# Performance work log

Measured on AMD Instinct MI355X. Metric: run time of the kernel, lower is better.

## Reference

```python
import jax, jax.numpy as jnp
import numpy as np


def setup_inputs() -> dict:
    key = jax.random.key(0)
    ks = jax.random.split(key, 9)
    B, T, F_IN = 128, 2048, 32
    R, H, F_OUT = 256, 256, 32
    s = lambda k, shape, fan: jax.random.normal(k, shape, dtype=jnp.float32) * (1.0 / np.sqrt(fan))
    return {
        "input_seq": jax.random.normal(ks[0], (B, T, F_IN), dtype=jnp.float32),
        "enc_W": s(ks[1], (R, F_IN), F_IN),
        "enc_b": s(ks[2], (R,), F_IN),
        "W_ih": s(ks[3], (4 * H, R), H),
        "W_hh": s(ks[4], (4 * H, H), H),
        "b_ih": s(ks[5], (4 * H,), H),
        "b_hh": s(ks[6], (4 * H,), H),
        "dec_W": s(ks[7], (F_OUT, H), H),
        "dec_b": s(ks[8], (F_OUT,), H),
        "future_n": 64,
    }


def reference(input_seq, enc_W, enc_b, W_ih, W_hh, b_ih, b_hh, dec_W, dec_b, future_n):
    # Faithful to source: `state` is never updated inside the loop, so every
    # timestep applies the LSTMCell to the SAME initial state (eval: zeros).
    B, T, _ = input_seq.shape
    H = W_hh.shape[1]
    h0 = jnp.zeros((B, H), dtype=input_seq.dtype)
    c0 = jnp.zeros((B, H), dtype=input_seq.dtype)

    encoded = jnp.einsum('btf,rf->btr', input_seq, enc_W) + enc_b  # [B,T,R]
    # future steps all reuse the last encoded timestep
    last = jnp.broadcast_to(encoded[:, -1:, :], (B, future_n, encoded.shape[-1]))
    enc_full = jnp.concatenate([encoded, last], axis=1)  # [B, T+future_n, R]

    # LSTMCell gates (PyTorch order: i, f, g, o); state contribution is constant.
    state_gates = h0 @ W_hh.T + b_hh  # [B, 4H] (zeros state -> just b_hh)
    gates = jnp.einsum('btr,gr->btg', enc_full, W_ih) + b_ih + state_gates[:, None, :]
    i, f, g, o = jnp.split(gates, 4, axis=-1)
    c = jax.nn.sigmoid(f) * c0[:, None, :] + jax.nn.sigmoid(i) * jnp.tanh(g)
    h = jax.nn.sigmoid(o) * jnp.tanh(c)  # [B, T+future_n, H]

    return jnp.einsum('bth,oh->bto', h, dec_W) + dec_b
```

## Files before the change

kernel.cpp:

```cpp
#include <hip/hip_runtime.h>


typedef _Float16 f16x8 __attribute__((ext_vector_type(8)));
typedef _Float16 f16x4 __attribute__((ext_vector_type(4)));
typedef float    f32x4 __attribute__((ext_vector_type(4)));
typedef _Float16 hx2   __attribute__((ext_vector_type(2)));
typedef __fp16   pk16x2 __attribute__((ext_vector_type(2)));

#define T_IN 2048
#define TT   2112
#define FIN  32
#define FOUT 32

#define WS_FB_OFF   49152
#define WS_DECW_OFF 52224

union PkCast { pk16x2 p; hx2 h; unsigned u; };

__device__ __forceinline__ hx2 pk2(float a, float b) {
    PkCast c; c.p = __builtin_amdgcn_cvt_pkrtz(a, b); return c.h;
}
__device__ __forceinline__ hx2 splat(float v) {
    _Float16 h = (_Float16)v; return (hx2){h, h};
}
__device__ __forceinline__ hx2 pk_rcp(hx2 d, hx2 TWO) {
    union { hx2 h; unsigned u; } a, r;
    a.h = d;
    r.u = 0x78007800u - a.u;
    hx2 y = r.h;
    y = y * (TWO - d * y);
    y = y * (TWO - d * y);
    return y;
}

__global__ __launch_bounds__(256) void prep2(
    const float* __restrict__ enc_W, const float* __restrict__ enc_b,
    const float* __restrict__ W_ih, const float* __restrict__ b_ih,
    const float* __restrict__ b_hh, const float* __restrict__ dec_W,
    _Float16* __restrict__ Mb, float* __restrict__ fb, _Float16* __restrict__ decWb) {
    const int blk = blockIdx.x;
    const int tid = threadIdx.x;
    if (blk < 768) {
        const int gg = blk, sg = gg + (gg >= 256 ? 256 : 0);
        const float scale = (gg >= 256 && gg < 512) ? 0.25f : 0.125f;
        const float* wr = W_ih + (size_t)sg * 256;
        const int f = tid & 31, r8 = tid >> 5;
        float acc = 0.f;
#pragma unroll
        for (int k = 0; k < 32; ++k) {
            int r = r8 * 32 + k;
            acc = fmaf(wr[r], enc_W[r * 32 + f], acc);
        }
        __shared__ float red[256];
        __shared__ float redb[256];
        __shared__ float red2[32];
        red[tid]  = acc;
        redb[tid] = wr[tid] * enc_b[tid];
        __syncthreads();
        if (tid < 32) {
            float s = 0.f;
#pragma unroll
            for (int k = 0; k < 8; ++k) s += red[k * 32 + tid];
            Mb[gg * 32 + tid] = (_Float16)(s * scale);
        } else if (tid >= 128 && tid < 160) {
            int t2 = tid - 128;
            float s2 = 0.f;
#pragma unroll
            for (int k = 0; k < 8; ++k) s2 += redb[t2 * 8 + k];
            red2[t2] = s2;
        }
        __syncthreads();
        if (tid == 0) {
            float t = b_ih[sg] + b_hh[sg];
#pragma unroll
            for (int k = 0; k < 32; ++k) t += red2[k];
            fb[gg] = t * scale;
        }
    } else {
        int i = (blk - 768) * 1024 + tid * 4;
        f32x4 v = *(const f32x4*)(dec_W + i);
        f16x4 o;
#pragma unroll
        for (int j = 0; j < 4; ++j) o[j] = (_Float16)v[j];
        *(f16x4*)(decWb + i) = o;
    }
}

__global__ __launch_bounds__(256) void lstm_main(
    const float* __restrict__ in, const _Float16* __restrict__ Mb,
    const float* __restrict__ fb, const _Float16* __restrict__ decWb,
    const float* __restrict__ dec_b, float* __restrict__ out) {
    __shared__ _Float16 hbuf[4][2][16 * 40];

    const int lane = threadIdx.x & 63;
    const int w    = threadIdx.x >> 6;
    const int l16  = lane & 15;
    const int q    = lane >> 4;
    const int wave = blockIdx.x * 4 + w;
    const int rowbase = wave * 32;
    const int b  = rowbase / TT;
    const int t0 = rowbase - b * TT;

    const hx2 C0 = splat(4.0f),      C1 = splat(7.757576f), C2 = splat(2.068687f);
    const hx2 D1 = splat(7.272727f), D2 = splat(5.171717f), D3 = splat(0.394036f);
    const hx2 ONE = splat(1.0f), H05 = splat(0.5f), TWO = splat(2.0f);
    const hx2 T0 = splat(0.99980f), T1 = splat(-0.32806f),
              T2 = splat(0.11306f), T3 = splat(-0.02344f);

    f16x8 bfr[2];
#pragma unroll
    for (int s = 0; s < 2; ++s) {
        int t  = t0 + s * 16 + l16;
        int tr = t < T_IN ? t : (T_IN - 1);
        const float* p = in + ((size_t)(b * T_IN + tr)) * FIN + q * 8;
        f32x4 u0 = *(const f32x4*)(p);
        f32x4 u1 = *(const f32x4*)(p + 4);
        union { hx2 h[4]; f16x8 v; } pk;
        pk.h[0] = pk2(u0[0], u0[1]); pk.h[1] = pk2(u0[2], u0[3]);
        pk.h[2] = pk2(u1[0], u1[1]); pk.h[3] = pk2(u1[2], u1[3]);
        bfr[s] = pk.v;
    }

    f32x4 dacc[2][2];
#pragma unroll
    for (int ot = 0; ot < 2; ++ot) {
        f32x4 db = *(const f32x4*)(dec_b + ot * 16 + q * 4);
        dacc[0][ot] = db; dacc[1][ot] = db;
    }

    for (int hc = 0; hc < 8; ++hc) {
        const int hb = hc * 32;
        f16x8 afr[3][2];
        f32x4 fbv[3][2];
#pragma unroll
        for (int gt = 0; gt < 3; ++gt)
#pragma unroll
            for (int X = 0; X < 2; ++X) {
                int grow = gt * 256 + hb + X * 16;
                afr[gt][X] = *(const f16x8*)(Mb + (size_t)(grow + l16) * 32 + q * 8);
                fbv[gt][X] = *(const f32x4*)(fb + grow + q * 4);
            }
        f16x8 a2[2];
#pragma unroll
        for (int ot = 0; ot < 2; ++ot)
            a2[ot] = *(const f16x8*)(decWb + (size_t)(ot * 16 + l16) * 256 + hb + q * 8);

#pragma unroll
        for (int s = 0; s < 2; ++s) {
            f32x4 gi[2], gg[2], go[2];
#pragma unroll
            for (int X = 0; X < 2; ++X) {
                gi[X] = __builtin_amdgcn_mfma_f32_16x16x32_f16(afr[0][X], bfr[s], fbv[0][X], 0, 0, 0);
                gg[X] = __builtin_amdgcn_mfma_f32_16x16x32_f16(afr[1][X], bfr[s], fbv[1][X], 0, 0, 0);
                go[X] = __builtin_amdgcn_mfma_f32_16x16x32_f16(afr[2][X], bfr[s], fbv[2][X], 0, 0, 0);
            }
            _Float16* hp = &hbuf[w][s][0];
#pragma unroll
            for (int X = 0; X < 2; ++X) {
                hx2 hpair[2];
#pragma unroll
                for (int p = 0; p < 2; ++p) {
                    hx2 ui = pk2(__builtin_amdgcn_fmed3f(gi[X][2*p],   -1.f, 1.f),
                                 __builtin_amdgcn_fmed3f(gi[X][2*p+1], -1.f, 1.f));
                    hx2 ug = pk2(__builtin_amdgcn_fmed3f(gg[X][2*p],   -1.f, 1.f),
                                 __builtin_amdgcn_fmed3f(gg[X][2*p+1], -1.f, 1.f));
                    hx2 uo = pk2(__builtin_amdgcn_fmed3f(go[X][2*p],   -1.f, 1.f),
                                 __builtin_amdgcn_fmed3f(go[X][2*p+1], -1.f, 1.f));
                    hx2 wi = ui * ui, wg = ug * ug, wo = uo * uo;
                    hx2 ni = ui * (wi * (wi * C2 + C1) + C0);
                    hx2 ng = ug * (wg * (wg * C2 + C1) + C0);
                    hx2 no = uo * (wo * (wo * C2 + C1) + C0);
                    hx2 di = wi * (wi * (wi * D3 + D2) + D1) + ONE;
                    hx2 dg = wg * (wg * (wg * D3 + D2) + D1) + ONE;
                    hx2 dd = wo * (wo * (wo * D3 + D2) + D1) + ONE;
                    hx2 ti = ni * pk_rcp(di, TWO);
                    hx2 tg = ng * pk_rcp(dg, TWO);
                    hx2 to = no * pk_rcp(dd, TWO);
                    hx2 si = ti * H05 + H05;
                    hx2 so = to * H05 + H05;
                    hx2 c  = si * tg;
                    hx2 z  = c * c;
                    hx2 P  = z * (z * (z * T3 + T2) + T1) + T0;
                    hpair[p] = so * (c * P);
                }
                union { hx2 h[2]; uint2 u; } hw;
                hw.h[0] = hpair[0]; hw.h[1] = hpair[1];
                *(uint2*)(hp + l16 * 40 + X * 16 + q * 4) = hw.u;
            }
            asm volatile("s_waitcnt lgkmcnt(0)" ::: "memory");
            f16x8 b2 = *(const f16x8*)(hp + l16 * 40 + q * 8);
#pragma unroll
            for (int ot = 0; ot < 2; ++ot)
                dacc[s][ot] = __builtin_amdgcn_mfma_f32_16x16x32_f16(a2[ot], b2, dacc[s][ot], 0, 0, 0);
        }
    }

#pragma unroll
    for (int s = 0; s < 2; ++s) {
        int t = t0 + s * 16 + l16;
        size_t ro = ((size_t)(b * TT + t)) * FOUT;
#pragma unroll
        for (int ot = 0; ot < 2; ++ot)
            *(f32x4*)(out + ro + ot * 16 + q * 4) = dacc[s][ot];
    }
}

extern "C" void kernel_launch(void* const* d_in, const int* in_sizes, int n_in,
                              void* d_out, int out_size, void* d_ws, size_t ws_size,
                              hipStream_t stream) {
    const float* input = (const float*)d_in[0];
    const float* enc_W = (const float*)d_in[1];
    const float* enc_b = (const float*)d_in[2];
    const float* W_ih  = (const float*)d_in[3];
    const float* b_ih  = (const float*)d_in[5];
    const float* b_hh  = (const float*)d_in[6];
    const float* dec_W = (const float*)d_in[7];
    const float* dec_b = (const float*)d_in[8];

    _Float16* Mb    = (_Float16*)d_ws;
    float*    fb    = (float*)((char*)d_ws + WS_FB_OFF);
    _Float16* decWb = (_Float16*)((char*)d_ws + WS_DECW_OFF);
    float*    out   = (float*)d_out;

    prep2<<<776, 256, 0, stream>>>(enc_W, enc_b, W_ih, b_ih, b_hh, dec_W, Mb, fb, decWb);
    lstm_main<<<2112, 256, 0, stream>>>(input, Mb, fb, decWb, dec_b, out);
}
```

Before: 170.2 us.

## Feed gate MFMA outputs directly into decoder MFMA, removing LDS round-trip

The decoder GEMM is restructured so the activated h values in the gate MFMA accumulator layout are used directly as the A operand of a 16x16x16 MFMA. Decoder weights are pre-permuted in the prep kernel to match, and the output is now the transposed accumulator. This drops the per-step LDS write, waitcnt and LDS read of the hidden tile. In exchange it issues twice as many smaller MFMAs and replaces the vectorized float4 output stores with scalar stores that are less coalesced.

```diff
diff --git a/kernel.cpp b/kernel.cpp
--- a/kernel.cpp
+++ b/kernel.cpp
@@ -37,7 +37,7 @@
     const float* __restrict__ enc_W, const float* __restrict__ enc_b,
     const float* __restrict__ W_ih, const float* __restrict__ b_ih,
     const float* __restrict__ b_hh, const float* __restrict__ dec_W,
-    _Float16* __restrict__ Mb, float* __restrict__ fb, _Float16* __restrict__ decWb) {
+    _Float16* __restrict__ Mb, float* __restrict__ fb, _Float16* __restrict__ decWb2) {
     const int blk = blockIdx.x;
     const int tid = threadIdx.x;
     if (blk < 768) {
@@ -77,21 +77,22 @@
             fb[gg] = t * scale;
         }
     } else {
-        int i = (blk - 768) * 1024 + tid * 4;
-        f32x4 v = *(const f32x4*)(dec_W + i);
+        int e4 = (blk - 768) * 256 + tid;
+        int od = e4 & 31, rest = e4 >> 5;
+        int q = rest & 3, kc = rest >> 2;
+        const float* src = dec_W + od * 256 + kc * 16 + 4 * q;
+        f32x4 v = *(const f32x4*)src;
         f16x4 o;
 #pragma unroll
         for (int j = 0; j < 4; ++j) o[j] = (_Float16)v[j];
-        *(f16x4*)(decWb + i) = o;
+        *(f16x4*)(decWb2 + (size_t)e4 * 4) = o;
     }
 }
 
 __global__ __launch_bounds__(256) void lstm_main(
     const float* __restrict__ in, const _Float16* __restrict__ Mb,
-    const float* __restrict__ fb, const _Float16* __restrict__ decWb,
+    const float* __restrict__ fb, const _Float16* __restrict__ decWb2,
     const float* __restrict__ dec_b, float* __restrict__ out) {
-    __shared__ _Float16 hbuf[4][2][16 * 40];
-
     const int lane = threadIdx.x & 63;
     const int w    = threadIdx.x >> 6;
     const int l16  = lane & 15;
@@ -124,8 +125,9 @@
     f32x4 dacc[2][2];
 #pragma unroll
     for (int ot = 0; ot < 2; ++ot) {
-        f32x4 db = *(const f32x4*)(dec_b + ot * 16 + q * 4);
-        dacc[0][ot] = db; dacc[1][ot] = db;
+        float db = dec_b[ot * 16 + l16];
+        f32x4 dv = {db, db, db, db};
+        dacc[0][ot] = dv; dacc[1][ot] = dv;
     }
 
     for (int hc = 0; hc < 8; ++hc) {
@@ -140,10 +142,15 @@
                 afr[gt][X] = *(const f16x8*)(Mb + (size_t)(grow + l16) * 32 + q * 8);
                 fbv[gt][X] = *(const f32x4*)(fb + grow + q * 4);
             }
-        f16x8 a2[2];
-#pragma unroll
-        for (int ot = 0; ot < 2; ++ot)
-            a2[ot] = *(const f16x8*)(decWb + (size_t)(ot * 16 + l16) * 256 + hb + q * 8);
+        f16x4 b2w[2][2];
+#pragma unroll
+        for (int X = 0; X < 2; ++X) {
+            int kc = 2 * hc + X;
+#pragma unroll
+            for (int ot = 0; ot < 2; ++ot)
+                b2w[X][ot] = *(const f16x4*)(decWb2 +
+                    (size_t)(((kc * 4 + q) * 32 + ot * 16 + l16)) * 4);
+        }
 
 #pragma unroll
         for (int s = 0; s < 2; ++s) {
@@ -154,7 +161,6 @@
                 gg[X] = __builtin_amdgcn_mfma_f32_16x16x32_f16(afr[1][X], bfr[s], fbv[1][X], 0, 0, 0);
                 go[X] = __builtin_amdgcn_mfma_f32_16x16x32_f16(afr[2][X], bfr[s], fbv[2][X], 0, 0, 0);
             }
-            _Float16* hp = &hbuf[w][s][0];
 #pragma unroll
             for (int X = 0; X < 2; ++X) {
                 hx2 hpair[2];
@@ -183,25 +189,27 @@
                     hx2 P  = z * (z * (z * T3 + T2) + T1) + T0;
                     hpair[p] = so * (c * P);
                 }
-                union { hx2 h[2]; uint2 u; } hw;
-                hw.h[0] = hpair[0]; hw.h[1] = hpair[1];
-                *(uint2*)(hp + l16 * 40 + X * 16 + q * 4) = hw.u;
-            }
-            asm volatile("s_waitcnt lgkmcnt(0)" ::: "memory");
-            f16x8 b2 = *(const f16x8*)(hp + l16 * 40 + q * 8);
-#pragma unroll
-            for (int ot = 0; ot < 2; ++ot)
-                dacc[s][ot] = __builtin_amdgcn_mfma_f32_16x16x32_f16(a2[ot], b2, dacc[s][ot], 0, 0, 0);
+                union { hx2 h[2]; f16x4 v; } a2f;
+                a2f.h[0] = hpair[0]; a2f.h[1] = hpair[1];
+#pragma unroll
+                for (int ot = 0; ot < 2; ++ot)
+                    dacc[s][ot] = __builtin_amdgcn_mfma_f32_16x16x16f16(
+                        a2f.v, b2w[X][ot], dacc[s][ot], 0, 0, 0);
+            }
         }
     }
 
 #pragma unroll
     for (int s = 0; s < 2; ++s) {
-        int t = t0 + s * 16 + l16;
-        size_t ro = ((size_t)(b * TT + t)) * FOUT;
-#pragma unroll
-        for (int ot = 0; ot < 2; ++ot)
-            *(f32x4*)(out + ro + ot * 16 + q * 4) = dacc[s][ot];
+#pragma unroll
+        for (int ot = 0; ot < 2; ++ot) {
+            f32x4 v = dacc[s][ot];
+#pragma unroll
+            for (int r = 0; r < 4; ++r) {
+                int t = t0 + s * 16 + 4 * q + r;
+                out[((size_t)(b * TT + t)) * FOUT + ot * 16 + l16] = v[r];
+            }
+        }
     }
 }
 
@@ -217,11 +225,11 @@
     const float* dec_W = (const float*)d_in[7];
     const float* dec_b = (const float*)d_in[8];
 
-    _Float16* Mb    = (_Float16*)d_ws;
-    float*    fb    = (float*)((char*)d_ws + WS_FB_OFF);
-    _Float16* decWb = (_Float16*)((char*)d_ws + WS_DECW_OFF);
-    float*    out   = (float*)d_out;
-
-    prep2<<<776, 256, 0, stream>>>(enc_W, enc_b, W_ih, b_ih, b_hh, dec_W, Mb, fb, decWb);
-    lstm_main<<<2112, 256, 0, stream>>>(input, Mb, fb, decWb, dec_b, out);
-}
+    _Float16* Mb     = (_Float16*)d_ws;
+    float*    fb     = (float*)((char*)d_ws + WS_FB_OFF);
+    _Float16* decWb2 = (_Float16*)((char*)d_ws + WS_DECW_OFF);
+    float*    out    = (float*)d_out;
+
+    prep2<<<776, 256, 0, stream>>>(enc_W, enc_b, W_ih, b_ih, b_hh, dec_W, Mb, fb, decWb2);
+    lstm_main<<<2112, 256, 0, stream>>>(input, Mb, fb, decWb2, dec_b, out);
+}
```

New measurement: 173.5 us. No clear change (+1.9%).
